# Performance work log

Hardware: AMD Instinct MI355X
Metric: run time of the kernel (lower is better)

Reference implementation:

```python
import jax, jax.numpy as jnp
import numpy as np

N, E, D, L = 50000, 800000, 128, 2
NEG_SLOPE = 0.2
LN_EPS = 1e-5


def setup_inputs() -> dict:
    key = jax.random.key(0)
    ks = jax.random.split(key, 6)
    scale = 1.0 / np.sqrt(D)
    x = jax.random.normal(ks[0], (N, D), dtype=jnp.float32)
    edge_index = jax.random.randint(ks[1], (2, E), 0, N, dtype=jnp.int64)
    W = jax.random.normal(ks[2], (L, D, D), dtype=jnp.float32) * scale
    att_src = jax.random.normal(ks[3], (L, D), dtype=jnp.float32) * scale
    att_dst = jax.random.normal(ks[4], (L, D), dtype=jnp.float32) * scale
    bias = jnp.zeros((L, D), dtype=jnp.float32)
    gamma = jnp.ones((L, D), dtype=jnp.float32)
    beta = jnp.zeros((L, D), dtype=jnp.float32)
    return {"x": x, "edge_index": edge_index, "W": W, "att_src": att_src,
            "att_dst": att_dst, "bias": bias, "gamma": gamma, "beta": beta}


def reference(x, edge_index, W, att_src, att_dst, bias, gamma, beta):
    # PyG GATConv (heads=1, concat=True, add_self_loops=True), eval mode
    # (attention/feature dropout disabled), followed by residual + LayerNorm.
    n = x.shape[0]
    loops = jnp.arange(n, dtype=edge_index.dtype)
    ei = jnp.concatenate([edge_index, jnp.stack([loops, loops])], axis=1)
    src, dst = ei[0], ei[1]  # messages flow src -> dst
    for l in range(W.shape[0]):
        h = x @ W[l]                              # [N, D]
        a_src = h @ att_src[l]                    # [N]
        a_dst = h @ att_dst[l]                    # [N]
        logit = jax.nn.leaky_relu(a_src[src] + a_dst[dst], NEG_SLOPE)  # [E+N]
        # segment softmax over incoming edges of each dst node
        m = jax.ops.segment_max(logit, dst, num_segments=n)
        e = jnp.exp(logit - m[dst])
        s = jax.ops.segment_sum(e, dst, num_segments=n)
        alpha = e / s[dst]
        msg = h[src] * alpha[:, None]             # [E+N, D]
        x_att = jax.ops.segment_sum(msg, dst, num_segments=n) + bias[l]
        # residual + LayerNorm
        y = x + x_att
        mu = jnp.mean(y, axis=-1, keepdims=True)
        var = jnp.var(y, axis=-1, keepdims=True)
        x = (y - mu) * jax.lax.rsqrt(var + LN_EPS) * gamma[l] + beta[l]
    return x
```

## Files before the change

kernel.cpp:

```cpp
#include <hip/hip_runtime.h>
#include <hip/hip_fp16.h>

#define D 128
#define NSLOPE 0.2f
#define LN_EPS 1e-5f
#define CAP 6144

typedef unsigned int uint;
typedef float f32x4 __attribute__((ext_vector_type(4)));
typedef _Float16 f16x8 __attribute__((ext_vector_type(8)));

__device__ __forceinline__ float leaky(float x) { return x > 0.f ? x : NSLOPE * x; }
__device__ __forceinline__ uint pkh(float a, float b) {
    __half2 h = __floats2half2_rn(a, b);
    return *reinterpret_cast<uint*>(&h);
}
__device__ __forceinline__ float2 h2f(uint u) {
    __half2 h = *reinterpret_cast<__half2*>(&u);
    return __half22float2(h);
}

__global__ void k_ginit(int* __restrict__ gcur, int nbuck) {
    int t = threadIdx.x;
    if (t < nbuck) gcur[t] = t * CAP;
}

__global__ __launch_bounds__(256) void k_bucket(const int* __restrict__ ei,
        int* __restrict__ gcur, uint* __restrict__ staging, int e, int nbuck) {
    __shared__ uint pr[4096];
    __shared__ int hist[256], gbase[256], c2[256];
    int t = threadIdx.x;
    int base = blockIdx.x * 4096;
    hist[t] = 0;
    c2[t] = 0;
    int nv = min(4096, e - base);
    for (int j = t; j < nv; j += 256) {
        int i = base + j;
        pr[j] = ((uint)ei[e + i] << 16) | (uint)ei[i];
    }
    __syncthreads();
    for (int j = t; j < nv; j += 256)
        atomicAdd(&hist[pr[j] >> 24], 1);
    __syncthreads();
    if (t < nbuck && hist[t] > 0) gbase[t] = atomicAdd(&gcur[t], hist[t]);
    __syncthreads();
    for (int j = t; j < nv; j += 256) {
        uint p = pr[j];
        int b = p >> 24;
        int pos = atomicAdd(&c2[b], 1);
        staging[gbase[b] + pos] = p;
    }
}

__global__ __launch_bounds__(256) void k_bdeg(const uint* __restrict__ staging,
        const int* __restrict__ gcur, int* __restrict__ deg,
        int* __restrict__ bsum, int n) {
    __shared__ int h[256];
    __shared__ int ws[4];
    int b = blockIdx.x, t = threadIdx.x;
    h[t] = 0;
    __syncthreads();
    int cnt = gcur[b] - b * CAP;
    for (int i = t; i < cnt; i += 256)
        atomicAdd(&h[(staging[b * CAP + i] >> 16) & 255], 1);
    __syncthreads();
    int node = b * 256 + t;
    int s = h[t];
    if (node < n) deg[node] = s;
    #pragma unroll
    for (int off = 32; off; off >>= 1) s += __shfl_xor(s, off);
    if ((t & 63) == 0) ws[t >> 6] = s;
    __syncthreads();
    if (t == 0) bsum[b] = ws[0] + ws[1] + ws[2] + ws[3];
}

__global__ __launch_bounds__(256) void k_scanb(const int* __restrict__ bsum,
        int* __restrict__ ebsum, int* __restrict__ rowptr_n, int nb) {
    __shared__ int lds[256];
    int t = threadIdx.x;
    int v = (t < nb) ? bsum[t] : 0;
    lds[t] = v;
    __syncthreads();
    for (int off = 1; off < 256; off <<= 1) {
        int u = (t >= off) ? lds[t - off] : 0;
        __syncthreads();
        lds[t] += u;
        __syncthreads();
    }
    if (t < nb) ebsum[t] = lds[t] - v;
    if (t == 255) *rowptr_n = lds[255];
}

__global__ __launch_bounds__(256) void k_rowptr(const int* __restrict__ deg,
        const int* __restrict__ ebsum, int* __restrict__ rowptr, int n) {
    __shared__ int lds[256];
    int b = blockIdx.x, t = threadIdx.x;
    int node = b * 256 + t;
    int d = (node < n) ? deg[node] : 0;
    lds[t] = d;
    __syncthreads();
    for (int off = 1; off < 256; off <<= 1) {
        int u = (t >= off) ? lds[t - off] : 0;
        __syncthreads();
        lds[t] += u;
        __syncthreads();
    }
    if (node < n) rowptr[node] = ebsum[b] + lds[t] - d;
}

__global__ __launch_bounds__(256) void k_bfill(const uint* __restrict__ staging,
        const int* __restrict__ gcur, const int* __restrict__ rowptr,
        int* __restrict__ csr, int n) {
    __shared__ int c2[256];
    int b = blockIdx.x, t = threadIdx.x;
    c2[t] = 0;
    __syncthreads();
    int cnt = gcur[b] - b * CAP;
    for (int i = t; i < cnt; i += 256) {
        uint p = staging[b * CAP + i];
        int d = p >> 16;
        int r = atomicAdd(&c2[d & 255], 1);
        csr[rowptr[d] + r] = (int)(p & 0xffffu);
    }
}

__global__ __launch_bounds__(256) void k_wt(const float* __restrict__ W,
                                            uint* __restrict__ wth) {
    __shared__ float T[128][17];
    int t = threadIdx.x;
    int c0 = blockIdx.x * 16;
    #pragma unroll
    for (int pass = 0; pass < 2; ++pass) {
        int k = pass * 64 + (t >> 2);
        int c = (t & 3) * 4;
        float4 v = *(const float4*)&W[k * D + c0 + c];
        T[k][c] = v.x; T[k][c + 1] = v.y; T[k][c + 2] = v.z; T[k][c + 3] = v.w;
    }
    __syncthreads();
    int cw = t >> 4;
    int k0 = (t & 15) * 8;
    uint4 uh;
    uh.x = pkh(T[k0 + 0][cw], T[k0 + 1][cw]);
    uh.y = pkh(T[k0 + 2][cw], T[k0 + 3][cw]);
    uh.z = pkh(T[k0 + 4][cw], T[k0 + 5][cw]);
    uh.w = pkh(T[k0 + 6][cw], T[k0 + 7][cw]);
    *(uint4*)&wth[(c0 + cw) * 64 + (t & 15) * 4] = uh;
}

__global__ __launch_bounds__(256) void k_gemm2(const float* __restrict__ x,
        const uint* __restrict__ wth, const float* __restrict__ avs,
        const float* __restrict__ avd, uint* __restrict__ hb,
        float* __restrict__ asrc, float* __restrict__ adst, int n) {
    __shared__ char XH[64 * 256];
    __shared__ char WH[128 * 256];
    __shared__ float psL[256], pdL[256];

    int t = threadIdx.x;
    int brow = blockIdx.x * 64;
    int rows = min(64, n - brow);

    #pragma unroll
    for (int i = 0; i < 8; ++i) {
        int f = t + 256 * i;
        int row = f >> 5, k4 = f & 31;
        float4 v = make_float4(0.f, 0.f, 0.f, 0.f);
        if (row < rows) v = *(const float4*)&x[(size_t)(brow + row) * D + k4 * 4];
        uint2 ph = make_uint2(pkh(v.x, v.y), pkh(v.z, v.w));
        int off = row * 256 + k4 * 8;
        int swz = (row & 7) << 4;
        *(uint2*)(XH + (off ^ swz)) = ph;
    }
    #pragma unroll
    for (int i = 0; i < 8; ++i) {
        int f = t + 256 * i;
        int col = f >> 4, j = f & 15;
        uint4 vh = *(const uint4*)&wth[col * 64 + j * 4];
        int off = col * 256 + j * 16;
        int swz = (col & 7) << 4;
        *(uint4*)(WH + (off ^ swz)) = vh;
    }
    __syncthreads();

    int wave = t >> 6, lane = t & 63;
    int l15 = lane & 15, lk = lane >> 4;

    f32x4 acc[4][2];
    #pragma unroll
    for (int rt = 0; rt < 4; ++rt)
        #pragma unroll
        for (int ct = 0; ct < 2; ++ct)
            acc[rt][ct] = (f32x4){0.f, 0.f, 0.f, 0.f};

    #pragma unroll
    for (int ks = 0; ks < 4; ++ks) {
        f16x8 a[4], b[2];
        #pragma unroll
        for (int rt = 0; rt < 4; ++rt) {
            int row = rt * 16 + l15;
            int off = row * 256 + (ks * 32 + lk * 8) * 2;
            int swz = (row & 7) << 4;
            a[rt] = *(const f16x8*)(XH + (off ^ swz));
        }
        #pragma unroll
        for (int ct = 0; ct < 2; ++ct) {
            int col = wave * 32 + ct * 16 + l15;
            int off = col * 256 + (ks * 32 + lk * 8) * 2;
            int swz = (col & 7) << 4;
            b[ct] = *(const f16x8*)(WH + (off ^ swz));
        }
        #pragma unroll
        for (int rt = 0; rt < 4; ++rt)
            #pragma unroll
            for (int ct = 0; ct < 2; ++ct)
                acc[rt][ct] = __builtin_amdgcn_mfma_f32_16x16x32_f16(a[rt], b[ct], acc[rt][ct], 0, 0, 0);
    }

    float avs_lo = avs[wave * 32 + l15], avs_hi = avs[wave * 32 + 16 + l15];
    float avd_lo = avd[wave * 32 + l15], avd_hi = avd[wave * 32 + 16 + l15];
    #pragma unroll
    for (int rt = 0; rt < 4; ++rt) {
        #pragma unroll
        for (int j = 0; j < 4; ++j) {
            float ps = acc[rt][0][j] * avs_lo + acc[rt][1][j] * avs_hi;
            float pd = acc[rt][0][j] * avd_lo + acc[rt][1][j] * avd_hi;
            #pragma unroll
            for (int off = 8; off; off >>= 1) {
                ps += __shfl_xor(ps, off);
                pd += __shfl_xor(pd, off);
            }
            int row = rt * 16 + lk * 4 + j;
            if (l15 == 0) { psL[wave * 64 + row] = ps; pdL[wave * 64 + row] = pd; }
        }
    }
    #pragma unroll
    for (int rt = 0; rt < 4; ++rt) {
        #pragma unroll
        for (int j = 0; j < 4; ++j) {
            int row = rt * 16 + lk * 4 + j;
            if (row < rows)
                hb[(size_t)(brow + row) * 64 + wave * 16 + l15] =
                    pkh(acc[rt][0][j], acc[rt][1][j]);
        }
    }
    __syncthreads();
    if (t < 64 && t < rows) {
        asrc[brow + t] = psL[t] + psL[64 + t] + psL[128 + t] + psL[192 + t];
        adst[brow + t] = pdL[t] + pdL[64 + t] + pdL[128 + t] + pdL[192 + t];
    }
}

__global__ __launch_bounds__(256) void k_attn(const float* __restrict__ x,
        const uint* __restrict__ hb, const float* __restrict__ asrc,
        const float* __restrict__ adst, const int* __restrict__ rowptr,
        const int* __restrict__ csr, const float* __restrict__ bias,
        const float* __restrict__ gamma, const float* __restrict__ beta,
        float* __restrict__ out, int n) {
    int node = blockIdx.x * 4 + (threadIdx.x >> 6);
    if (node >= n) return;
    int lane = threadIdx.x & 63;
    int grp = lane >> 4;
    int sl = lane & 15;
    int base_lo = (sl >> 2) * 32 + (sl & 3) * 4;

    float a_i = adst[node];
    float slg = leaky(asrc[node] + a_i);
    int rs = rowptr[node], re = rowptr[node + 1];

    float m_g, ssum;
    float acc[8];
    if (grp == 0) {
        m_g = slg; ssum = 1.f;
        uint4 q = *(const uint4*)&hb[(size_t)node * 64 + sl * 4];
        float2 f0 = h2f(q.x), f1 = h2f(q.y), f2 = h2f(q.z), f3 = h2f(q.w);
        acc[0] = f0.x; acc[1] = f1.x; acc[2] = f2.x; acc[3] = f3.x;
        acc[4] = f0.y; acc[5] = f1.y; acc[6] = f2.y; acc[7] = f3.y;
    } else {
        m_g = -1e30f; ssum = 0.f;
        #pragma unroll
        for (int j = 0; j < 8; ++j) acc[j] = 0.f;
    }

    for (int e = rs; e < re; e += 8) {
        int e0 = e + grp, e1 = e + 4 + grp;
        int c0 = min(e0, re - 1), c1 = min(e1, re - 1);
        int s0 = csr[c0], s1 = csr[c1];
        uint4 q0 = *(const uint4*)&hb[(size_t)s0 * 64 + sl * 4];
        uint4 q1 = *(const uint4*)&hb[(size_t)s1 * 64 + sl * 4];
        float lg0 = (e0 < re) ? leaky(asrc[s0] + a_i) : -1e30f;
        float lg1 = (e1 < re) ? leaky(asrc[s1] + a_i) : -1e30f;
        float nm = fmaxf(m_g, fmaxf(lg0, lg1));
        if (nm > m_g) {
            float sc = __expf(m_g - nm);
            ssum *= sc;
            #pragma unroll
            for (int j = 0; j < 8; ++j) acc[j] *= sc;
            m_g = nm;
        }
        float w0 = (e0 < re) ? __expf(lg0 - nm) : 0.f;
        float w1 = (e1 < re) ? __expf(lg1 - nm) : 0.f;
        ssum += w0 + w1;
        float2 a0 = h2f(q0.x), a1 = h2f(q0.y), a2 = h2f(q0.z), a3 = h2f(q0.w);
        float2 b0 = h2f(q1.x), b1 = h2f(q1.y), b2 = h2f(q1.z), b3 = h2f(q1.w);
        acc[0] += w0 * a0.x + w1 * b0.x;
        acc[1] += w0 * a1.x + w1 * b1.x;
        acc[2] += w0 * a2.x + w1 * b2.x;
        acc[3] += w0 * a3.x + w1 * b3.x;
        acc[4] += w0 * a0.y + w1 * b0.y;
        acc[5] += w0 * a1.y + w1 * b1.y;
        acc[6] += w0 * a2.y + w1 * b2.y;
        acc[7] += w0 * a3.y + w1 * b3.y;
    }

    float m = m_g;
    #pragma unroll
    for (int off = 16; off <= 32; off <<= 1) m = fmaxf(m, __shfl_xor(m, off));
    float sc = __expf(m_g - m);
    ssum *= sc;
    #pragma unroll
    for (int j = 0; j < 8; ++j) acc[j] *= sc;
    #pragma unroll
    for (int off = 16; off <= 32; off <<= 1) {
        ssum += __shfl_xor(ssum, off);
        #pragma unroll
        for (int j = 0; j < 8; ++j) acc[j] += __shfl_xor(acc[j], off);
    }
    float inv = 1.f / ssum;

    float4 xa = *(const float4*)&x[(size_t)node * D + base_lo];
    float4 xb = *(const float4*)&x[(size_t)node * D + base_lo + 16];
    float4 ba = *(const float4*)&bias[base_lo];
    float4 bb = *(const float4*)&bias[base_lo + 16];
    float y[8];
    y[0] = xa.x + acc[0] * inv + ba.x;
    y[1] = xa.y + acc[1] * inv + ba.y;
    y[2] = xa.z + acc[2] * inv + ba.z;
    y[3] = xa.w + acc[3] * inv + ba.w;
    y[4] = xb.x + acc[4] * inv + bb.x;
    y[5] = xb.y + acc[5] * inv + bb.y;
    y[6] = xb.z + acc[6] * inv + bb.z;
    y[7] = xb.w + acc[7] * inv + bb.w;

    float s1 = 0.f, s2 = 0.f;
    #pragma unroll
    for (int j = 0; j < 8; ++j) { s1 += y[j]; s2 += y[j] * y[j]; }
    #pragma unroll
    for (int off = 1; off <= 8; off <<= 1) {
        s1 += __shfl_xor(s1, off);
        s2 += __shfl_xor(s2, off);
    }
    float mu = s1 * (1.f / D);
    float var = s2 * (1.f / D) - mu * mu;
    float rstd = rsqrtf(var + LN_EPS);

    if (grp == 0) {
        float4 ga = *(const float4*)&gamma[base_lo];
        float4 gb = *(const float4*)&gamma[base_lo + 16];
        float4 bta = *(const float4*)&beta[base_lo];
        float4 btb = *(const float4*)&beta[base_lo + 16];
        float4 o0, o1;
        o0.x = (y[0] - mu) * rstd * ga.x + bta.x;
        o0.y = (y[1] - mu) * rstd * ga.y + bta.y;
        o0.z = (y[2] - mu) * rstd * ga.z + bta.z;
        o0.w = (y[3] - mu) * rstd * ga.w + bta.w;
        o1.x = (y[4] - mu) * rstd * gb.x + btb.x;
        o1.y = (y[5] - mu) * rstd * gb.y + btb.y;
        o1.z = (y[6] - mu) * rstd * gb.z + btb.z;
        o1.w = (y[7] - mu) * rstd * gb.w + btb.w;
        *(float4*)&out[(size_t)node * D + base_lo] = o0;
        *(float4*)&out[(size_t)node * D + base_lo + 16] = o1;
    }
}

extern "C" void kernel_launch(void* const* d_in, const int* in_sizes, int n_in,
                              void* d_out, int out_size, void* d_ws, size_t ws_size,
                              hipStream_t stream) {
    const float* x       = (const float*)d_in[0];
    const int*   ei      = (const int*)d_in[1];
    const float* W       = (const float*)d_in[2];
    const float* att_src = (const float*)d_in[3];
    const float* att_dst = (const float*)d_in[4];
    const float* bias    = (const float*)d_in[5];
    const float* gamma   = (const float*)d_in[6];
    const float* beta    = (const float*)d_in[7];
    float* out = (float*)d_out;

    const int N = in_sizes[0] / D;
    const int E = in_sizes[1] / 2;
    const int L = in_sizes[2] / (D * D);
    const int NBUCK = (N + 255) / 256;

    char* base = (char*)d_ws;
    size_t off = 0;
    auto alloc = [&](size_t bytes) {
        char* p = base + off;
        off += (bytes + 255) & ~(size_t)255;
        return p;
    };
    uint*  hb      = (uint*)alloc((size_t)N * 64 * 4);
    float* asrc    = (float*)alloc((size_t)N * 4);
    float* adst    = (float*)alloc((size_t)N * 4);
    int*   deg     = (int*)alloc((size_t)N * 4);
    int*   rowptr  = (int*)alloc((size_t)(N + 1) * 4);
    int*   csr     = (int*)alloc((size_t)E * 4);
    uint*  staging = (uint*)alloc((size_t)NBUCK * CAP * 4);
    int*   gcur    = (int*)alloc((size_t)NBUCK * 4);
    int*   bsum    = (int*)alloc((size_t)NBUCK * 4);
    int*   ebsum   = (int*)alloc((size_t)NBUCK * 4);
    uint*  wth     = (uint*)alloc((size_t)D * 64 * 4);

    k_ginit<<<1, 256, 0, stream>>>(gcur, NBUCK);
    k_bucket<<<(E + 4095) / 4096, 256, 0, stream>>>(ei, gcur, staging, E, NBUCK);
    k_bdeg<<<NBUCK, 256, 0, stream>>>(staging, gcur, deg, bsum, N);
    k_scanb<<<1, 256, 0, stream>>>(bsum, ebsum, rowptr + N, NBUCK);
    k_rowptr<<<NBUCK, 256, 0, stream>>>(deg, ebsum, rowptr, N);
    k_bfill<<<NBUCK, 256, 0, stream>>>(staging, gcur, rowptr, csr, N);

    const int nblk_node = (N + 3) / 4;
    for (int l = 0; l < L; ++l) {
        const float* xl = (l == 0) ? x : out;
        k_wt<<<8, 256, 0, stream>>>(W + (size_t)l * D * D, wth);
        k_gemm2<<<(N + 63) / 64, 256, 0, stream>>>(xl, wth,
                                                   att_src + (size_t)l * D,
                                                   att_dst + (size_t)l * D,
                                                   hb, asrc, adst, N);
        k_attn<<<nblk_node, 256, 0, stream>>>(xl, hb, asrc, adst, rowptr, csr,
                                              bias + (size_t)l * D, gamma + (size_t)l * D,
                                              beta + (size_t)l * D, out, N);
    }
}
```

Before: 166.9 us.

## Use fp16 intermediate activations, half2 accumulation, and merge scan kernels

New measurement: 164.5 us. No clear change (-1.4%).

```diff
diff --git a/kernel.cpp b/kernel.cpp
--- a/kernel.cpp
+++ b/kernel.cpp
@@ -18,6 +18,9 @@
 __device__ __forceinline__ float2 h2f(uint u) {
     __half2 h = *reinterpret_cast<__half2*>(&u);
     return __half22float2(h);
+}
+__device__ __forceinline__ __half2 u2h2(uint u) {
+    return *reinterpret_cast<__half2*>(&u);
 }
 
 __global__ void k_ginit(int* __restrict__ gcur, int nbuck) {
@@ -74,12 +77,23 @@
     if (t == 0) bsum[b] = ws[0] + ws[1] + ws[2] + ws[3];
 }
 
-__global__ __launch_bounds__(256) void k_scanb(const int* __restrict__ bsum,
-        int* __restrict__ ebsum, int* __restrict__ rowptr_n, int nb) {
+__global__ __launch_bounds__(256) void k_rowptr(const int* __restrict__ deg,
+        const int* __restrict__ bsum, int* __restrict__ rowptr, int n, int nb) {
+    __shared__ int sb[256];
     __shared__ int lds[256];
-    int t = threadIdx.x;
-    int v = (t < nb) ? bsum[t] : 0;
-    lds[t] = v;
+    int b = blockIdx.x, t = threadIdx.x;
+    sb[t] = (t < nb) ? bsum[t] : 0;
+    __syncthreads();
+    for (int off = 1; off < 256; off <<= 1) {
+        int u = (t >= off) ? sb[t - off] : 0;
+        __syncthreads();
+        sb[t] += u;
+        __syncthreads();
+    }
+    int ebase = (b == 0) ? 0 : sb[b - 1];
+    int node = b * 256 + t;
+    int d = (node < n) ? deg[node] : 0;
+    lds[t] = d;
     __syncthreads();
     for (int off = 1; off < 256; off <<= 1) {
         int u = (t >= off) ? lds[t - off] : 0;
@@ -87,25 +101,8 @@
         lds[t] += u;
         __syncthreads();
     }
-    if (t < nb) ebsum[t] = lds[t] - v;
-    if (t == 255) *rowptr_n = lds[255];
-}
-
-__global__ __launch_bounds__(256) void k_rowptr(const int* __restrict__ deg,
-        const int* __restrict__ ebsum, int* __restrict__ rowptr, int n) {
-    __shared__ int lds[256];
-    int b = blockIdx.x, t = threadIdx.x;
-    int node = b * 256 + t;
-    int d = (node < n) ? deg[node] : 0;
-    lds[t] = d;
-    __syncthreads();
-    for (int off = 1; off < 256; off <<= 1) {
-        int u = (t >= off) ? lds[t - off] : 0;
-        __syncthreads();
-        lds[t] += u;
-        __syncthreads();
-    }
-    if (node < n) rowptr[node] = ebsum[b] + lds[t] - d;
+    if (node < n) rowptr[node] = ebase + lds[t] - d;
+    if (b == gridDim.x - 1 && t == 0) rowptr[n] = sb[nb - 1];
 }
 
 __global__ __launch_bounds__(256) void k_bfill(const uint* __restrict__ staging,
@@ -147,10 +144,11 @@
     *(uint4*)&wth[(c0 + cw) * 64 + (t & 15) * 4] = uh;
 }
 
-__global__ __launch_bounds__(256) void k_gemm2(const float* __restrict__ x,
-        const uint* __restrict__ wth, const float* __restrict__ avs,
-        const float* __restrict__ avd, uint* __restrict__ hb,
-        float* __restrict__ asrc, float* __restrict__ adst, int n) {
+template <bool F16IN>
+__global__ __launch_bounds__(256) void k_gemm2(const float* __restrict__ xf,
+        const uint* __restrict__ xh, const uint* __restrict__ wth,
+        const float* __restrict__ avs, const float* __restrict__ avd,
+        uint* __restrict__ hb, float* __restrict__ asrc, float* __restrict__ adst, int n) {
     __shared__ char XH[64 * 256];
     __shared__ char WH[128 * 256];
     __shared__ float psL[256], pdL[256];
@@ -163,9 +161,15 @@
     for (int i = 0; i < 8; ++i) {
         int f = t + 256 * i;
         int row = f >> 5, k4 = f & 31;
-        float4 v = make_float4(0.f, 0.f, 0.f, 0.f);
-        if (row < rows) v = *(const float4*)&x[(size_t)(brow + row) * D + k4 * 4];
-        uint2 ph = make_uint2(pkh(v.x, v.y), pkh(v.z, v.w));
+        uint2 ph = make_uint2(0u, 0u);
+        if (row < rows) {
+            if (F16IN) {
+                ph = *(const uint2*)&xh[(size_t)(brow + row) * 64 + k4 * 2];
+            } else {
+                float4 v = *(const float4*)&xf[(size_t)(brow + row) * D + k4 * 4];
+                ph = make_uint2(pkh(v.x, v.y), pkh(v.z, v.w));
+            }
+        }
         int off = row * 256 + k4 * 8;
         int swz = (row & 7) << 4;
         *(uint2*)(XH + (off ^ swz)) = ph;
@@ -249,12 +253,14 @@
     }
 }
 
-__global__ __launch_bounds__(256) void k_attn(const float* __restrict__ x,
-        const uint* __restrict__ hb, const float* __restrict__ asrc,
-        const float* __restrict__ adst, const int* __restrict__ rowptr,
-        const int* __restrict__ csr, const float* __restrict__ bias,
-        const float* __restrict__ gamma, const float* __restrict__ beta,
-        float* __restrict__ out, int n) {
+template <int MODE>
+__global__ __launch_bounds__(256) void k_attn(const float* __restrict__ xf,
+        const uint* __restrict__ xh, const uint* __restrict__ hb,
+        const float* __restrict__ asrc, const float* __restrict__ adst,
+        const int* __restrict__ rowptr, const int* __restrict__ csr,
+        const float* __restrict__ bias, const float* __restrict__ gamma,
+        const float* __restrict__ beta, float* __restrict__ out,
+        uint* __restrict__ outh, int n) {
     int node = blockIdx.x * 4 + (threadIdx.x >> 6);
     if (node >= n) return;
     int lane = threadIdx.x & 63;
@@ -267,17 +273,17 @@
     int rs = rowptr[node], re = rowptr[node + 1];
 
     float m_g, ssum;
-    float acc[8];
+    __half2 acch[4];
     if (grp == 0) {
         m_g = slg; ssum = 1.f;
         uint4 q = *(const uint4*)&hb[(size_t)node * 64 + sl * 4];
-        float2 f0 = h2f(q.x), f1 = h2f(q.y), f2 = h2f(q.z), f3 = h2f(q.w);
-        acc[0] = f0.x; acc[1] = f1.x; acc[2] = f2.x; acc[3] = f3.x;
-        acc[4] = f0.y; acc[5] = f1.y; acc[6] = f2.y; acc[7] = f3.y;
+        acch[0] = u2h2(q.x); acch[1] = u2h2(q.y);
+        acch[2] = u2h2(q.z); acch[3] = u2h2(q.w);
     } else {
         m_g = -1e30f; ssum = 0.f;
-        #pragma unroll
-        for (int j = 0; j < 8; ++j) acc[j] = 0.f;
+        __half2 z = __half2half2(__float2half(0.f));
+        #pragma unroll
+        for (int j = 0; j < 4; ++j) acch[j] = z;
     }
 
     for (int e = rs; e < re; e += 8) {
@@ -292,23 +298,24 @@
         if (nm > m_g) {
             float sc = __expf(m_g - nm);
             ssum *= sc;
+            __half2 sch = __half2half2(__float2half(sc));
             #pragma unroll
-            for (int j = 0; j < 8; ++j) acc[j] *= sc;
+            for (int j = 0; j < 4; ++j) acch[j] = __hmul2(acch[j], sch);
             m_g = nm;
         }
         float w0 = (e0 < re) ? __expf(lg0 - nm) : 0.f;
         float w1 = (e1 < re) ? __expf(lg1 - nm) : 0.f;
         ssum += w0 + w1;
-        float2 a0 = h2f(q0.x), a1 = h2f(q0.y), a2 = h2f(q0.z), a3 = h2f(q0.w);
-        float2 b0 = h2f(q1.x), b1 = h2f(q1.y), b2 = h2f(q1.z), b3 = h2f(q1.w);
-        acc[0] += w0 * a0.x + w1 * b0.x;
-        acc[1] += w0 * a1.x + w1 * b1.x;
-        acc[2] += w0 * a2.x + w1 * b2.x;
-        acc[3] += w0 * a3.x + w1 * b3.x;
-        acc[4] += w0 * a0.y + w1 * b0.y;
-        acc[5] += w0 * a1.y + w1 * b1.y;
-        acc[6] += w0 * a2.y + w1 * b2.y;
-        acc[7] += w0 * a3.y + w1 * b3.y;
+        __half2 w0h = __half2half2(__float2half(w0));
+        __half2 w1h = __half2half2(__float2half(w1));
+        acch[0] = __hfma2(w0h, u2h2(q0.x), acch[0]);
+        acch[1] = __hfma2(w0h, u2h2(q0.y), acch[1]);
+        acch[2] = __hfma2(w0h, u2h2(q0.z), acch[2]);
+        acch[3] = __hfma2(w0h, u2h2(q0.w), acch[3]);
+        acch[0] = __hfma2(w1h, u2h2(q1.x), acch[0]);
+        acch[1] = __hfma2(w1h, u2h2(q1.y), acch[1]);
+        acch[2] = __hfma2(w1h, u2h2(q1.z), acch[2]);
+        acch[3] = __hfma2(w1h, u2h2(q1.w), acch[3]);
     }
 
     float m = m_g;
@@ -316,8 +323,15 @@
     for (int off = 16; off <= 32; off <<= 1) m = fmaxf(m, __shfl_xor(m, off));
     float sc = __expf(m_g - m);
     ssum *= sc;
-    #pragma unroll
-    for (int j = 0; j < 8; ++j) acc[j] *= sc;
+    float acc[8];
+    {
+        float2 f0 = __half22float2(acch[0]);
+        float2 f1 = __half22float2(acch[1]);
+        float2 f2 = __half22float2(acch[2]);
+        float2 f3 = __half22float2(acch[3]);
+        acc[0] = f0.x * sc; acc[1] = f1.x * sc; acc[2] = f2.x * sc; acc[3] = f3.x * sc;
+        acc[4] = f0.y * sc; acc[5] = f1.y * sc; acc[6] = f2.y * sc; acc[7] = f3.y * sc;
+    }
     #pragma unroll
     for (int off = 16; off <= 32; off <<= 1) {
         ssum += __shfl_xor(ssum, off);
@@ -326,19 +340,30 @@
     }
     float inv = 1.f / ssum;
 
-    float4 xa = *(const float4*)&x[(size_t)node * D + base_lo];
-    float4 xb = *(const float4*)&x[(size_t)node * D + base_lo + 16];
+    float x0, x1, x2, x3, x4, x5, x6, x7;
+    if (MODE == 0) {
+        float4 xa = *(const float4*)&xf[(size_t)node * D + base_lo];
+        float4 xb = *(const float4*)&xf[(size_t)node * D + base_lo + 16];
+        x0 = xa.x; x1 = xa.y; x2 = xa.z; x3 = xa.w;
+        x4 = xb.x; x5 = xb.y; x6 = xb.z; x7 = xb.w;
+    } else {
+        uint2 ua = *(const uint2*)&xh[(size_t)node * 64 + (base_lo >> 1)];
+        uint2 ub = *(const uint2*)&xh[(size_t)node * 64 + (base_lo >> 1) + 8];
+        float2 fa0 = h2f(ua.x), fa1 = h2f(ua.y), fb0 = h2f(ub.x), fb1 = h2f(ub.y);
+        x0 = fa0.x; x1 = fa0.y; x2 = fa1.x; x3 = fa1.y;
+        x4 = fb0.x; x5 = fb0.y; x6 = fb1.x; x7 = fb1.y;
+    }
     float4 ba = *(const float4*)&bias[base_lo];
     float4 bb = *(const float4*)&bias[base_lo + 16];
     float y[8];
-    y[0] = xa.x + acc[0] * inv + ba.x;
-    y[1] = xa.y + acc[1] * inv + ba.y;
-    y[2] = xa.z + acc[2] * inv + ba.z;
-    y[3] = xa.w + acc[3] * inv + ba.w;
-    y[4] = xb.x + acc[4] * inv + bb.x;
-    y[5] = xb.y + acc[5] * inv + bb.y;
-    y[6] = xb.z + acc[6] * inv + bb.z;
-    y[7] = xb.w + acc[7] * inv + bb.w;
+    y[0] = x0 + acc[0] * inv + ba.x;
+    y[1] = x1 + acc[1] * inv + ba.y;
+    y[2] = x2 + acc[2] * inv + ba.z;
+    y[3] = x3 + acc[3] * inv + ba.w;
+    y[4] = x4 + acc[4] * inv + bb.x;
+    y[5] = x5 + acc[5] * inv + bb.y;
+    y[6] = x6 + acc[6] * inv + bb.z;
+    y[7] = x7 + acc[7] * inv + bb.w;
 
     float s1 = 0.f, s2 = 0.f;
     #pragma unroll
@@ -357,17 +382,23 @@
         float4 gb = *(const float4*)&gamma[base_lo + 16];
         float4 bta = *(const float4*)&beta[base_lo];
         float4 btb = *(const float4*)&beta[base_lo + 16];
-        float4 o0, o1;
-        o0.x = (y[0] - mu) * rstd * ga.x + bta.x;
-        o0.y = (y[1] - mu) * rstd * ga.y + bta.y;
-        o0.z = (y[2] - mu) * rstd * ga.z + bta.z;
-        o0.w = (y[3] - mu) * rstd * ga.w + bta.w;
-        o1.x = (y[4] - mu) * rstd * gb.x + btb.x;
-        o1.y = (y[5] - mu) * rstd * gb.y + btb.y;
-        o1.z = (y[6] - mu) * rstd * gb.z + btb.z;
-        o1.w = (y[7] - mu) * rstd * gb.w + btb.w;
-        *(float4*)&out[(size_t)node * D + base_lo] = o0;
-        *(float4*)&out[(size_t)node * D + base_lo + 16] = o1;
+        float o0 = (y[0] - mu) * rstd * ga.x + bta.x;
+        float o1 = (y[1] - mu) * rstd * ga.y + bta.y;
+        float o2 = (y[2] - mu) * rstd * ga.z + bta.z;
+        float o3 = (y[3] - mu) * rstd * ga.w + bta.w;
+        float o4 = (y[4] - mu) * rstd * gb.x + btb.x;
+        float o5 = (y[5] - mu) * rstd * gb.y + btb.y;
+        float o6 = (y[6] - mu) * rstd * gb.z + btb.z;
+        float o7 = (y[7] - mu) * rstd * gb.w + btb.w;
+        if (MODE == 0) {
+            uint2 oa = make_uint2(pkh(o0, o1), pkh(o2, o3));
+            uint2 ob = make_uint2(pkh(o4, o5), pkh(o6, o7));
+            *(uint2*)&outh[(size_t)node * 64 + (base_lo >> 1)] = oa;
+            *(uint2*)&outh[(size_t)node * 64 + (base_lo >> 1) + 8] = ob;
+        } else {
+            *(float4*)&out[(size_t)node * D + base_lo] = make_float4(o0, o1, o2, o3);
+            *(float4*)&out[(size_t)node * D + base_lo + 16] = make_float4(o4, o5, o6, o7);
+        }
     }
 }
 
@@ -386,7 +417,6 @@
 
     const int N = in_sizes[0] / D;
     const int E = in_sizes[1] / 2;
-    const int L = in_sizes[2] / (D * D);
     const int NBUCK = (N + 255) / 256;
 
     char* base = (char*)d_ws;
@@ -397,6 +427,7 @@
         return p;
     };
     uint*  hb      = (uint*)alloc((size_t)N * 64 * 4);
+    uint*  xh16    = (uint*)alloc((size_t)N * 64 * 4);
     float* asrc    = (float*)alloc((size_t)N * 4);
     float* adst    = (float*)alloc((size_t)N * 4);
     int*   deg     = (int*)alloc((size_t)N * 4);
@@ -405,26 +436,26 @@
     uint*  staging = (uint*)alloc((size_t)NBUCK * CAP * 4);
     int*   gcur    = (int*)alloc((size_t)NBUCK * 4);
     int*   bsum    = (int*)alloc((size_t)NBUCK * 4);
-    int*   ebsum   = (int*)alloc((size_t)NBUCK * 4);
     uint*  wth     = (uint*)alloc((size_t)D * 64 * 4);
 
     k_ginit<<<1, 256, 0, stream>>>(gcur, NBUCK);
     k_bucket<<<(E + 4095) / 4096, 256, 0, stream>>>(ei, gcur, staging, E, NBUCK);
     k_bdeg<<<NBUCK, 256, 0, stream>>>(staging, gcur, deg, bsum, N);
-    k_scanb<<<1, 256, 0, stream>>>(bsum, ebsum, rowptr + N, NBUCK);
-    k_rowptr<<<NBUCK, 256, 0, stream>>>(deg, ebsum, rowptr, N);
+    k_rowptr<<<NBUCK, 256, 0, stream>>>(deg, bsum, rowptr, N, NBUCK);
     k_bfill<<<NBUCK, 256, 0, stream>>>(staging, gcur, rowptr, csr, N);
 
     const int nblk_node = (N + 3) / 4;
-    for (int l = 0; l < L; ++l) {
-        const float* xl = (l == 0) ? x : out;
-        k_wt<<<8, 256, 0, stream>>>(W + (size_t)l * D * D, wth);
-        k_gemm2<<<(N + 63) / 64, 256, 0, stream>>>(xl, wth,
-                                                   att_src + (size_t)l * D,
-                                                   att_dst + (size_t)l * D,
-                                                   hb, asrc, adst, N);
-        k_attn<<<nblk_node, 256, 0, stream>>>(xl, hb, asrc, adst, rowptr, csr,
-                                              bias + (size_t)l * D, gamma + (size_t)l * D,
-                                              beta + (size_t)l * D, out, N);
-    }
-}
+    const int nblk_gemm = (N + 63) / 64;
+
+    k_wt<<<8, 256, 0, stream>>>(W, wth);
+    k_gemm2<false><<<nblk_gemm, 256, 0, stream>>>(x, nullptr, wth, att_src, att_dst,
+                                                  hb, asrc, adst, N);
+    k_attn<0><<<nblk_node, 256, 0, stream>>>(x, nullptr, hb, asrc, adst, rowptr, csr,
+                                             bias, gamma, beta, nullptr, xh16, N);
+    k_wt<<<8, 256, 0, stream>>>(W + (size_t)D * D, wth);
+    k_gemm2<true><<<nblk_gemm, 256, 0, stream>>>(nullptr, xh16, wth,
+                                                 att_src + D, att_dst + D,
+                                                 hb, asrc, adst, N);
+    k_attn<1><<<nblk_node, 256, 0, stream>>>(nullptr, xh16, hb, asrc, adst, rowptr, csr,
+                                             bias + D, gamma + D, beta + D, out, nullptr, N);
+}
```
